# Optimization experiments

Measured on AMD Instinct MI355X. Metric: run time of the kernel, lower is better.

## Reference

```python
import jax, jax.numpy as jnp
import numpy as np

B, S, D = 8, 2048, 768        # batch, seq_len, embed_dim
G1, G2, G3 = 16, 16, 16       # grid_shape
L = 768                       # latent_dim
TEMP = 0.5                    # initial temperature (learnable scalar)
GRID_STD = 0.05               # keras 'random_normal' default stddev


def _glorot_uniform(key, fan_in, fan_out):
    lim = jnp.sqrt(6.0 / (fan_in + fan_out))
    return jax.random.uniform(key, (fan_in, fan_out), minval=-lim, maxval=lim, dtype=jnp.float32)


def setup_inputs() -> dict:
    key = jax.random.key(0)
    kx, k1, k2, k3, kg = jax.random.split(key, 5)
    x = jax.random.normal(kx, (B, S, D), dtype=jnp.float32)
    W1 = _glorot_uniform(k1, D, G1)
    W2 = _glorot_uniform(k2, D, G2)
    W3 = _glorot_uniform(k3, D, G3)
    b1 = jnp.zeros((G1,), jnp.float32)
    b2 = jnp.zeros((G2,), jnp.float32)
    b3 = jnp.zeros((G3,), jnp.float32)
    grid = GRID_STD * jax.random.normal(kg, (G1, G2, G3, L), dtype=jnp.float32)
    temperature = jnp.asarray(TEMP, dtype=jnp.float32)
    return {"x": x, "W1": W1, "b1": b1, "W2": W2, "b2": b2,
            "W3": W3, "b3": b3, "grid": grid, "temperature": temperature}


def reference(x, W1, b1, W2, b2, W3, b3, grid, temperature):
    # Flatten (batch, seq) -> tokens, process each token independently (transformer mode)
    b, s, d = x.shape
    xt = x.reshape(b * s, d)                                # (T, D)
    # Per-dimension temperature-controlled softmax addressing distributions
    p1 = jax.nn.softmax((xt @ W1 + b1) / temperature, axis=-1)   # (T, G1)
    p2 = jax.nn.softmax((xt @ W2 + b2) / temperature, axis=-1)   # (T, G2)
    p3 = jax.nn.softmax((xt @ W3 + b3) / temperature, axis=-1)   # (T, G3)
    # Joint probability (outer product) contracted with grid latent vectors:
    # out[t, l] = sum_{i,j,k} p1[t,i] p2[t,j] p3[t,k] grid[i,j,k,l]
    out = jnp.einsum('ti,tj,tk,ijkl->tl', p1, p2, p3, grid, optimize=True)
    return out.reshape(b, s, -1)                            # (B, S, L)
```

## Files before the change

kernel.cpp:

```cpp
#include <hip/hip_runtime.h>
#include <hip/hip_bf16.h>


using short8 = __attribute__((ext_vector_type(8))) short;
using f32x4  = __attribute__((ext_vector_type(4))) float;
using f32x16 = __attribute__((ext_vector_type(16))) float;
using half8  = __attribute__((ext_vector_type(8))) _Float16;
using half2v = __attribute__((ext_vector_type(2))) _Float16;
typedef unsigned short ushort_t;
typedef unsigned int uint_t;

typedef const __attribute__((address_space(1))) void* gptr_t;
typedef __attribute__((address_space(3))) void* lptr_t;

#define PSTRIDE 52

static __device__ __forceinline__ ushort_t f2h_bits(float x) {
  union { _Float16 h; ushort_t u; } c;
  c.h = (_Float16)x;
  return c.u;
}

static __device__ __forceinline__ half2v cvt_pkrtz2(float a, float b) {
  auto r = __builtin_amdgcn_cvt_pkrtz(a, b);
  union { decltype(r) i; half2v o; } u;
  u.i = r;
  return u.o;
}

__global__ __launch_bounds__(512) void k_pre(const float* __restrict__ g,
                                             ushort_t* __restrict__ gT,
                                             const float* __restrict__ x,
                                             const float* __restrict__ W1, const float* __restrict__ b1,
                                             const float* __restrict__ W2, const float* __restrict__ b2,
                                             const float* __restrict__ W3, const float* __restrict__ b3,
                                             const float* __restrict__ temp,
                                             float* __restrict__ p) {
  __shared__ union SmT {
    ushort_t tile[64][65];
    float x2[2][64][100];
    float partial[4][64][PSTRIDE];
  } sm;
  const int tid = threadIdx.x;
  const int bid = blockIdx.x;

  if (bid < 768) {
    const int r0 = (bid & 63) * 64;
    const int c0 = (bid >> 6) * 64;
#pragma unroll
    for (int it = 0; it < 2; ++it) {
      const int idx = tid + it * 512;
      const int r = idx >> 4;
      const int c = (idx & 15) << 2;
      const float4 v = *(const float4*)(g + (size_t)(r0 + r) * 768 + (c0 + c));
      sm.tile[c + 0][r] = f2h_bits(v.x);
      sm.tile[c + 1][r] = f2h_bits(v.y);
      sm.tile[c + 2][r] = f2h_bits(v.z);
      sm.tile[c + 3][r] = f2h_bits(v.w);
    }
    __syncthreads();
#pragma unroll
    for (int it = 0; it < 2; ++it) {
      const int idx = tid + it * 512;
      const int r = idx >> 4;
      const int c = (idx & 15) << 2;
      ushort4 o;
      o.x = sm.tile[r][c + 0]; o.y = sm.tile[r][c + 1];
      o.z = sm.tile[r][c + 2]; o.w = sm.tile[r][c + 3];
      *(ushort4*)(gT + (size_t)(c0 + r) * 4096 + (r0 + c)) = o;
    }
    return;
  }

  const int lane = tid & 63;
  const int wv = __builtin_amdgcn_readfirstlane(tid >> 6);
  const int t0 = (bid - 768) * 64;

  float acc[48];
#pragma unroll
  for (int q = 0; q < 48; ++q) acc[q] = 0.f;

  const float* xbase = x + (size_t)t0 * 768;
  auto load_chunk = [&](int c, int b) {
#pragma unroll
    for (int it = 0; it < 3; ++it) {
      const int q = tid + it * 512;
      const int r = q / 24;
      const int c4 = q % 24;
      const float4 v = *(const float4*)(xbase + (size_t)r * 768 + c * 96 + c4 * 4);
      *(float4*)&sm.x2[b][r][c4 * 4] = v;
    }
  };

  load_chunk(0, 0);
  __syncthreads();
  for (int c = 0; c < 8; ++c) {
    const int cur = c & 1;
    if (c < 7) load_chunk(c + 1, cur ^ 1);
    float xv[12];
#pragma unroll
    for (int rr = 0; rr < 3; ++rr) {
      const f32x4 v = *(const f32x4*)&sm.x2[cur][lane][wv * 12 + rr * 4];
      xv[rr * 4 + 0] = v[0]; xv[rr * 4 + 1] = v[1];
      xv[rr * 4 + 2] = v[2]; xv[rr * 4 + 3] = v[3];
    }
#pragma unroll
    for (int dd = 0; dd < 12; ++dd) {
      const int d = c * 96 + wv * 12 + dd;
      const float xs = xv[dd];
      const float* w1r = W1 + d * 16;
      const float* w2r = W2 + d * 16;
      const float* w3r = W3 + d * 16;
#pragma unroll
      for (int gg = 0; gg < 16; ++gg) {
        acc[gg]      = fmaf(xs, w1r[gg], acc[gg]);
        acc[16 + gg] = fmaf(xs, w2r[gg], acc[16 + gg]);
        acc[32 + gg] = fmaf(xs, w3r[gg], acc[32 + gg]);
      }
    }
    __syncthreads();
  }

  if (wv >= 4) {
    f32x4* dst = (f32x4*)sm.partial[wv - 4][lane];
#pragma unroll
    for (int q = 0; q < 12; ++q) dst[q] = *(const f32x4*)&acc[q * 4];
  }
  __syncthreads();
  if (wv < 4) {
    const f32x4* src = (const f32x4*)sm.partial[wv][lane];
#pragma unroll
    for (int q = 0; q < 12; ++q) {
      const f32x4 v = src[q];
#pragma unroll
      for (int e = 0; e < 4; ++e) acc[q * 4 + e] += v[e];
    }
  }
  __syncthreads();
  if (wv == 2 || wv == 3) {
    f32x4* dst = (f32x4*)sm.partial[wv - 2][lane];
#pragma unroll
    for (int q = 0; q < 12; ++q) dst[q] = *(const f32x4*)&acc[q * 4];
  }
  __syncthreads();
  if (wv < 2) {
    const f32x4* src = (const f32x4*)sm.partial[wv][lane];
#pragma unroll
    for (int q = 0; q < 12; ++q) {
      const f32x4 v = src[q];
#pragma unroll
      for (int e = 0; e < 4; ++e) acc[q * 4 + e] += v[e];
    }
  }
  __syncthreads();
  if (wv == 1) {
    f32x4* dst = (f32x4*)sm.partial[0][lane];
#pragma unroll
    for (int q = 0; q < 12; ++q) dst[q] = *(const f32x4*)&acc[q * 4];
  }
  __syncthreads();
  if (wv == 0) {
    const f32x4* src = (const f32x4*)sm.partial[0][lane];
#pragma unroll
    for (int q = 0; q < 12; ++q) {
      const f32x4 v = src[q];
#pragma unroll
      for (int e = 0; e < 4; ++e) acc[q * 4 + e] += v[e];
    }
    const float invT = 1.0f / temp[0];
    float* prow = p + (size_t)(t0 + lane) * PSTRIDE;
#pragma unroll
    for (int grp = 0; grp < 3; ++grp) {
      const float* bias = (grp == 0) ? b1 : (grp == 1) ? b2 : b3;
      float z[16];
      float m = -3.0e38f;
#pragma unroll
      for (int q = 0; q < 16; ++q) {
        z[q] = (acc[grp * 16 + q] + bias[q]) * invT;
        m = fmaxf(m, z[q]);
      }
      float s = 0.f;
#pragma unroll
      for (int q = 0; q < 16; ++q) { z[q] = __expf(z[q] - m); s += z[q]; }
      const float rs = 1.0f / s;
#pragma unroll
      for (int q = 0; q < 16; ++q) prow[grp * 16 + q] = z[q] * rs;
    }
  }
}

__global__ __launch_bounds__(256, 2) void k_gemm(const float* __restrict__ p_g,
                                                 const ushort_t* __restrict__ gT,
                                                 float* __restrict__ out) {
  __shared__ ushort_t Bt[2][192 * 64];
  __shared__ float p1T[16 * 128];

  const int tid = threadIdx.x;
  const int lane = tid & 63;
  const int wv = __builtin_amdgcn_readfirstlane(tid >> 6);
  const int wm = wv >> 1, wn = wv & 1;
  const int g = lane >> 5;
  const int l31 = lane & 31;

  const int f = blockIdx.y * 128 + blockIdx.x;
  const int w = (f & 7) * 64 + (f >> 3);
  const int m0 = (w & 127) * 128;
  const int n0 = (w >> 7) * 192;

  if (tid < 128) {
    const float* pr = p_g + (size_t)(m0 + tid) * PSTRIDE;
#pragma unroll
    for (int qq = 0; qq < 4; ++qq) {
      const f32x4 v = *(const f32x4*)(pr + qq * 4);
#pragma unroll
      for (int e = 0; e < 4; ++e) p1T[(qq * 4 + e) * 128 + tid] = v[e];
    }
  }

  const int rowA0 = m0 + wm * 64 + l31;
  half2v p2h[2][16];
  float p3r[2][8];
#pragma unroll
  for (int mr = 0; mr < 2; ++mr) {
    const float* pr = p_g + (size_t)(rowA0 + mr * 32) * PSTRIDE;
#pragma unroll
    for (int qq = 0; qq < 4; ++qq) {
      const f32x4 v = *(const f32x4*)(pr + 16 + qq * 4);
#pragma unroll
      for (int e = 0; e < 4; ++e)
        p2h[mr][qq * 4 + e] = cvt_pkrtz2(v[e], v[e]);
    }
#pragma unroll
    for (int qq = 0; qq < 2; ++qq) {
      const f32x4 v = *(const f32x4*)(pr + 32 + 8 * g + qq * 4);
      p3r[mr][qq * 4 + 0] = v[0]; p3r[mr][qq * 4 + 1] = v[1];
      p3r[mr][qq * 4 + 2] = v[2]; p3r[mr][qq * 4 + 3] = v[3];
    }
  }

  const int srow = wv * 48 + (lane >> 3);
  const int schunk = (lane & 7) ^ (lane >> 3);
  const ushort_t* sbase = gT + (size_t)(n0 + srow) * 4096 + schunk * 8;
  auto stage = [&](int buf, int kt) {
    const ushort_t* src = sbase + kt * 64;
#pragma unroll
    for (int q = 0; q < 6; ++q) {
      __builtin_amdgcn_global_load_lds((gptr_t)(src + (size_t)q * 8 * 4096),
                                       (lptr_t)&Bt[buf][(wv * 48 + q * 8) * 64], 16, 0, 0);
    }
  };

  f32x16 acc[2][3];
#pragma unroll
  for (int mr = 0; mr < 2; ++mr)
#pragma unroll
    for (int nf = 0; nf < 3; ++nf)
#pragma unroll
      for (int e = 0; e < 16; ++e) acc[mr][nf][e] = 0.f;

  stage(0, 0);
  asm volatile("s_waitcnt vmcnt(0) lgkmcnt(0)" ::: "memory");
  __builtin_amdgcn_s_barrier();

  const int rowLoc0 = wm * 64 + l31;
  for (int io = 0; io < 16; ++io) {
    half2v p1p3h[2][4];
#pragma unroll
    for (int mr = 0; mr < 2; ++mr) {
      const float p1v = p1T[io * 128 + rowLoc0 + mr * 32];
#pragma unroll
      for (int q = 0; q < 4; ++q)
        p1p3h[mr][q] = cvt_pkrtz2(p1v * p3r[mr][2 * q],
                                  p1v * p3r[mr][2 * q + 1]);
    }
#pragma unroll
    for (int kq = 0; kq < 4; ++kq) {
      const int kt = io * 4 + kq;
      const ushort_t* bbuf = Bt[kq & 1];

      half8 b[4][3];
#pragma unroll
      for (int s = 0; s < 4; ++s) {
        const int cd = 2 * s + g;
#pragma unroll
        for (int nf = 0; nf < 3; ++nf) {
          const int r = wn * 96 + nf * 32 + l31;
          b[s][nf] = *(const half8*)&bbuf[r * 64 + ((cd ^ (r & 7)) << 3)];
        }
      }
      if (kq < 3 || io < 15) stage((kq + 1) & 1, kt + 1);

#pragma unroll
      for (int s = 0; s < 4; ++s) {
        const int j = kq * 4 + s;
        half8 a[2];
#pragma unroll
        for (int mr = 0; mr < 2; ++mr) {
          union { half2v h2[4]; half8 h8; } pk;
#pragma unroll
          for (int q = 0; q < 4; ++q) pk.h2[q] = p2h[mr][j] * p1p3h[mr][q];
          a[mr] = pk.h8;
        }
        __builtin_amdgcn_s_setprio(1);
#pragma unroll
        for (int mr = 0; mr < 2; ++mr)
#pragma unroll
          for (int nf = 0; nf < 3; ++nf)
            acc[mr][nf] = __builtin_amdgcn_mfma_f32_32x32x16_f16(a[mr], b[s][nf], acc[mr][nf], 0, 0, 0);
        __builtin_amdgcn_s_setprio(0);
      }
      asm volatile("s_waitcnt vmcnt(0)" ::: "memory");
      __builtin_amdgcn_s_barrier();
    }
  }

#pragma unroll
  for (int mr = 0; mr < 2; ++mr)
#pragma unroll
    for (int nf = 0; nf < 3; ++nf)
#pragma unroll
      for (int reg = 0; reg < 16; ++reg) {
        const int row = (reg & 3) + 8 * (reg >> 2) + 4 * g;
        const int t = m0 + wm * 64 + mr * 32 + row;
        out[(size_t)t * 768 + n0 + wn * 96 + nf * 32 + l31] = acc[mr][nf][reg];
      }
}

extern "C" void kernel_launch(void* const* d_in, const int* in_sizes, int n_in,
                              void* d_out, int out_size, void* d_ws, size_t ws_size,
                              hipStream_t stream) {
  (void)in_sizes; (void)n_in; (void)out_size; (void)ws_size;
  const float* x    = (const float*)d_in[0];
  const float* W1   = (const float*)d_in[1];
  const float* b1   = (const float*)d_in[2];
  const float* W2   = (const float*)d_in[3];
  const float* b2   = (const float*)d_in[4];
  const float* W3   = (const float*)d_in[5];
  const float* b3   = (const float*)d_in[6];
  const float* grid = (const float*)d_in[7];
  const float* temp = (const float*)d_in[8];
  float* out = (float*)d_out;

  ushort_t* gT = (ushort_t*)d_ws;
  float* p = (float*)((char*)d_ws + 6291456);

  k_pre<<<dim3(1024), 512, 0, stream>>>(grid, gT, x, W1, b1, W2, b2, W3, b3, temp, p);
  k_gemm<<<dim3(128, 4), 256, 0, stream>>>(p, gT, out);
}
```

Before: 131.3 us.

## Triple-buffer B tiles with two-deep prefetch and vectorize projection FMAs

After: 150.3 us. +14.5%, slower.

```diff
diff --git a/kernel.cpp b/kernel.cpp
--- a/kernel.cpp
+++ b/kernel.cpp
@@ -3,6 +3,7 @@
 
 
 using short8 = __attribute__((ext_vector_type(8))) short;
+using f32x2  = __attribute__((ext_vector_type(2))) float;
 using f32x4  = __attribute__((ext_vector_type(4))) float;
 using f32x16 = __attribute__((ext_vector_type(16))) float;
 using half8  = __attribute__((ext_vector_type(8))) _Float16;
@@ -79,6 +80,7 @@
   float acc[48];
 #pragma unroll
   for (int q = 0; q < 48; ++q) acc[q] = 0.f;
+  f32x2* a2 = (f32x2*)acc;
 
   const float* xbase = x + (size_t)t0 * 768;
   auto load_chunk = [&](int c, int b) {
@@ -108,14 +110,15 @@
     for (int dd = 0; dd < 12; ++dd) {
       const int d = c * 96 + wv * 12 + dd;
       const float xs = xv[dd];
-      const float* w1r = W1 + d * 16;
-      const float* w2r = W2 + d * 16;
-      const float* w3r = W3 + d * 16;
-#pragma unroll
-      for (int gg = 0; gg < 16; ++gg) {
-        acc[gg]      = fmaf(xs, w1r[gg], acc[gg]);
-        acc[16 + gg] = fmaf(xs, w2r[gg], acc[16 + gg]);
-        acc[32 + gg] = fmaf(xs, w3r[gg], acc[32 + gg]);
+      const f32x2 xs2 = {xs, xs};
+      const f32x2* w1r = (const f32x2*)(W1 + d * 16);
+      const f32x2* w2r = (const f32x2*)(W2 + d * 16);
+      const f32x2* w3r = (const f32x2*)(W3 + d * 16);
+#pragma unroll
+      for (int gg = 0; gg < 8; ++gg) {
+        a2[gg]      = __builtin_elementwise_fma(xs2, w1r[gg], a2[gg]);
+        a2[8 + gg]  = __builtin_elementwise_fma(xs2, w2r[gg], a2[8 + gg]);
+        a2[16 + gg] = __builtin_elementwise_fma(xs2, w3r[gg], a2[16 + gg]);
       }
     }
     __syncthreads();
@@ -192,8 +195,8 @@
 __global__ __launch_bounds__(256, 2) void k_gemm(const float* __restrict__ p_g,
                                                  const ushort_t* __restrict__ gT,
                                                  float* __restrict__ out) {
-  __shared__ ushort_t Bt[2][192 * 64];
-  __shared__ float p1T[16 * 128];
+  __shared__ ushort_t Bt[3 * 192 * 64];
+  __shared__ ushort_t p1h[16 * 128];
 
   const int tid = threadIdx.x;
   const int lane = tid & 63;
@@ -213,7 +216,7 @@
     for (int qq = 0; qq < 4; ++qq) {
       const f32x4 v = *(const f32x4*)(pr + qq * 4);
 #pragma unroll
-      for (int e = 0; e < 4; ++e) p1T[(qq * 4 + e) * 128 + tid] = v[e];
+      for (int e = 0; e < 4; ++e) p1h[(qq * 4 + e) * 128 + tid] = f2h_bits(v[e]);
     }
   }
 
@@ -246,7 +249,7 @@
 #pragma unroll
     for (int q = 0; q < 6; ++q) {
       __builtin_amdgcn_global_load_lds((gptr_t)(src + (size_t)q * 8 * 4096),
-                                       (lptr_t)&Bt[buf][(wv * 48 + q * 8) * 64], 16, 0, 0);
+                                       (lptr_t)&Bt[buf * 12288 + (wv * 48 + q * 8) * 64], 16, 0, 0);
     }
   };
 
@@ -258,16 +261,24 @@
 #pragma unroll
       for (int e = 0; e < 16; ++e) acc[mr][nf][e] = 0.f;
 
-  stage(0, 0);
   asm volatile("s_waitcnt vmcnt(0) lgkmcnt(0)" ::: "memory");
   __builtin_amdgcn_s_barrier();
 
+  stage(0, 0);
+  stage(1, 1);
+  asm volatile("s_waitcnt vmcnt(6)" ::: "memory");
+  __builtin_amdgcn_s_barrier();
+
   const int rowLoc0 = wm * 64 + l31;
+  int bufc = 0;
+  int sbuf = 2;
   for (int io = 0; io < 16; ++io) {
     half2v p1p3h[2][4];
 #pragma unroll
     for (int mr = 0; mr < 2; ++mr) {
-      const float p1v = p1T[io * 128 + rowLoc0 + mr * 32];
+      union { ushort_t u; _Float16 h; } c;
+      c.u = p1h[io * 128 + rowLoc0 + mr * 32];
+      const float p1v = (float)c.h;
 #pragma unroll
       for (int q = 0; q < 4; ++q)
         p1p3h[mr][q] = cvt_pkrtz2(p1v * p3r[mr][2 * q],
@@ -276,8 +287,9 @@
 #pragma unroll
     for (int kq = 0; kq < 4; ++kq) {
       const int kt = io * 4 + kq;
-      const ushort_t* bbuf = Bt[kq & 1];
-
+      if (kt < 62) stage(sbuf, kt + 2);
+
+      const ushort_t* bbuf = &Bt[bufc * 12288];
       half8 b[4][3];
 #pragma unroll
       for (int s = 0; s < 4; ++s) {
@@ -288,7 +300,6 @@
           b[s][nf] = *(const half8*)&bbuf[r * 64 + ((cd ^ (r & 7)) << 3)];
         }
       }
-      if (kq < 3 || io < 15) stage((kq + 1) & 1, kt + 1);
 
 #pragma unroll
       for (int s = 0; s < 4; ++s) {
@@ -309,8 +320,15 @@
             acc[mr][nf] = __builtin_amdgcn_mfma_f32_32x32x16_f16(a[mr], b[s][nf], acc[mr][nf], 0, 0, 0);
         __builtin_amdgcn_s_setprio(0);
       }
-      asm volatile("s_waitcnt vmcnt(0)" ::: "memory");
-      __builtin_amdgcn_s_barrier();
+
+      if (kt < 62) {
+        asm volatile("s_waitcnt vmcnt(6)" ::: "memory");
+      } else if (kt == 62) {
+        asm volatile("s_waitcnt vmcnt(0)" ::: "memory");
+      }
+      if (kt < 63) __builtin_amdgcn_s_barrier();
+      bufc = (bufc == 2) ? 0 : bufc + 1;
+      sbuf = (sbuf == 2) ? 0 : sbuf + 1;
     }
   }
 
```

## Compute addressing logits with fp16 MFMA and split pre-pass into pack and prep kernels

Applied to the files above, without the earlier changes.

After: 106.6 us, median of 2. -18.8%, faster.

```diff
diff --git a/kernel.cpp b/kernel.cpp
--- a/kernel.cpp
+++ b/kernel.cpp
@@ -2,7 +2,7 @@
 #include <hip/hip_bf16.h>
 
 
-using short8 = __attribute__((ext_vector_type(8))) short;
+using f32x2  = __attribute__((ext_vector_type(2))) float;
 using f32x4  = __attribute__((ext_vector_type(4))) float;
 using f32x16 = __attribute__((ext_vector_type(16))) float;
 using half8  = __attribute__((ext_vector_type(8))) _Float16;
@@ -28,164 +28,126 @@
   return u.o;
 }
 
-__global__ __launch_bounds__(512) void k_pre(const float* __restrict__ g,
-                                             ushort_t* __restrict__ gT,
-                                             const float* __restrict__ x,
-                                             const float* __restrict__ W1, const float* __restrict__ b1,
-                                             const float* __restrict__ W2, const float* __restrict__ b2,
-                                             const float* __restrict__ W3, const float* __restrict__ b3,
-                                             const float* __restrict__ temp,
-                                             float* __restrict__ p) {
-  __shared__ union SmT {
-    ushort_t tile[64][65];
-    float x2[2][64][100];
-    float partial[4][64][PSTRIDE];
-  } sm;
+__global__ __launch_bounds__(256) void k_pack(const float* __restrict__ g,
+                                              ushort_t* __restrict__ gT,
+                                              const float* __restrict__ W1,
+                                              const float* __restrict__ W2,
+                                              const float* __restrict__ W3,
+                                              ushort_t* __restrict__ wfrag) {
+  const int tx = threadIdx.x;
+  if (blockIdx.y == 12) {
+    if (blockIdx.x >= 9) return;
+#pragma unroll
+    for (int j = 0; j < 16; ++j) {
+      const int u = blockIdx.x * 4096 + tx * 16 + j;
+      const int e = u & 7;
+      const int l = (u >> 3) & 63;
+      const int frag = u >> 9;
+      const int ks = frag / 3, nf = frag % 3;
+      const int d = ks * 32 + 8 * (l >> 4) + e;
+      const int col = l & 15;
+      const float* Wsel = (nf == 0) ? W1 : (nf == 1) ? W2 : W3;
+      wfrag[u] = f2h_bits(Wsel[d * 16 + col]);
+    }
+    return;
+  }
+  __shared__ ushort_t tile[64][65];
+  const int r0 = blockIdx.x * 64;
+  const int c0 = blockIdx.y * 64;
+#pragma unroll
+  for (int it = 0; it < 4; ++it) {
+    const int idx = tx + it * 256;
+    const int r = idx >> 4;
+    const int c = (idx & 15) << 2;
+    const float4 v = *(const float4*)(g + (size_t)(r0 + r) * 768 + (c0 + c));
+    tile[c + 0][r] = f2h_bits(v.x);
+    tile[c + 1][r] = f2h_bits(v.y);
+    tile[c + 2][r] = f2h_bits(v.z);
+    tile[c + 3][r] = f2h_bits(v.w);
+  }
+  __syncthreads();
+#pragma unroll
+  for (int it = 0; it < 4; ++it) {
+    const int idx = tx + it * 256;
+    const int r = idx >> 4;
+    const int c = (idx & 15) << 2;
+    ushort4 o;
+    o.x = tile[r][c + 0]; o.y = tile[r][c + 1];
+    o.z = tile[r][c + 2]; o.w = tile[r][c + 3];
+    *(ushort4*)(gT + (size_t)(c0 + r) * 4096 + (r0 + c)) = o;
+  }
+}
+
+__global__ __launch_bounds__(256) void k_prep(const float* __restrict__ x,
+                                              const ushort_t* __restrict__ wfrag,
+                                              const float* __restrict__ b1,
+                                              const float* __restrict__ b2,
+                                              const float* __restrict__ b3,
+                                              const float* __restrict__ temp,
+                                              float* __restrict__ p) {
   const int tid = threadIdx.x;
-  const int bid = blockIdx.x;
-
-  if (bid < 768) {
-    const int r0 = (bid & 63) * 64;
-    const int c0 = (bid >> 6) * 64;
-#pragma unroll
-    for (int it = 0; it < 2; ++it) {
-      const int idx = tid + it * 512;
-      const int r = idx >> 4;
-      const int c = (idx & 15) << 2;
-      const float4 v = *(const float4*)(g + (size_t)(r0 + r) * 768 + (c0 + c));
-      sm.tile[c + 0][r] = f2h_bits(v.x);
-      sm.tile[c + 1][r] = f2h_bits(v.y);
-      sm.tile[c + 2][r] = f2h_bits(v.z);
-      sm.tile[c + 3][r] = f2h_bits(v.w);
-    }
-    __syncthreads();
-#pragma unroll
-    for (int it = 0; it < 2; ++it) {
-      const int idx = tid + it * 512;
-      const int r = idx >> 4;
-      const int c = (idx & 15) << 2;
-      ushort4 o;
-      o.x = sm.tile[r][c + 0]; o.y = sm.tile[r][c + 1];
-      o.z = sm.tile[r][c + 2]; o.w = sm.tile[r][c + 3];
-      *(ushort4*)(gT + (size_t)(c0 + r) * 4096 + (r0 + c)) = o;
-    }
-    return;
-  }
-
   const int lane = tid & 63;
-  const int wv = __builtin_amdgcn_readfirstlane(tid >> 6);
-  const int t0 = (bid - 768) * 64;
-
-  float acc[48];
-#pragma unroll
-  for (int q = 0; q < 48; ++q) acc[q] = 0.f;
-
-  const float* xbase = x + (size_t)t0 * 768;
-  auto load_chunk = [&](int c, int b) {
-#pragma unroll
-    for (int it = 0; it < 3; ++it) {
-      const int q = tid + it * 512;
-      const int r = q / 24;
-      const int c4 = q % 24;
-      const float4 v = *(const float4*)(xbase + (size_t)r * 768 + c * 96 + c4 * 4);
-      *(float4*)&sm.x2[b][r][c4 * 4] = v;
-    }
-  };
-
-  load_chunk(0, 0);
-  __syncthreads();
-  for (int c = 0; c < 8; ++c) {
-    const int cur = c & 1;
-    if (c < 7) load_chunk(c + 1, cur ^ 1);
-    float xv[12];
-#pragma unroll
-    for (int rr = 0; rr < 3; ++rr) {
-      const f32x4 v = *(const f32x4*)&sm.x2[cur][lane][wv * 12 + rr * 4];
-      xv[rr * 4 + 0] = v[0]; xv[rr * 4 + 1] = v[1];
-      xv[rr * 4 + 2] = v[2]; xv[rr * 4 + 3] = v[3];
-    }
-#pragma unroll
-    for (int dd = 0; dd < 12; ++dd) {
-      const int d = c * 96 + wv * 12 + dd;
-      const float xs = xv[dd];
-      const float* w1r = W1 + d * 16;
-      const float* w2r = W2 + d * 16;
-      const float* w3r = W3 + d * 16;
-#pragma unroll
-      for (int gg = 0; gg < 16; ++gg) {
-        acc[gg]      = fmaf(xs, w1r[gg], acc[gg]);
-        acc[16 + gg] = fmaf(xs, w2r[gg], acc[16 + gg]);
-        acc[32 + gg] = fmaf(xs, w3r[gg], acc[32 + gg]);
-      }
-    }
-    __syncthreads();
-  }
-
-  if (wv >= 4) {
-    f32x4* dst = (f32x4*)sm.partial[wv - 4][lane];
-#pragma unroll
-    for (int q = 0; q < 12; ++q) dst[q] = *(const f32x4*)&acc[q * 4];
-  }
-  __syncthreads();
-  if (wv < 4) {
-    const f32x4* src = (const f32x4*)sm.partial[wv][lane];
-#pragma unroll
-    for (int q = 0; q < 12; ++q) {
-      const f32x4 v = src[q];
-#pragma unroll
-      for (int e = 0; e < 4; ++e) acc[q * 4 + e] += v[e];
-    }
-  }
-  __syncthreads();
-  if (wv == 2 || wv == 3) {
-    f32x4* dst = (f32x4*)sm.partial[wv - 2][lane];
-#pragma unroll
-    for (int q = 0; q < 12; ++q) dst[q] = *(const f32x4*)&acc[q * 4];
-  }
-  __syncthreads();
-  if (wv < 2) {
-    const f32x4* src = (const f32x4*)sm.partial[wv][lane];
-#pragma unroll
-    for (int q = 0; q < 12; ++q) {
-      const f32x4 v = src[q];
-#pragma unroll
-      for (int e = 0; e < 4; ++e) acc[q * 4 + e] += v[e];
-    }
-  }
-  __syncthreads();
-  if (wv == 1) {
-    f32x4* dst = (f32x4*)sm.partial[0][lane];
-#pragma unroll
-    for (int q = 0; q < 12; ++q) dst[q] = *(const f32x4*)&acc[q * 4];
-  }
-  __syncthreads();
-  if (wv == 0) {
-    const f32x4* src = (const f32x4*)sm.partial[0][lane];
-#pragma unroll
-    for (int q = 0; q < 12; ++q) {
-      const f32x4 v = src[q];
-#pragma unroll
-      for (int e = 0; e < 4; ++e) acc[q * 4 + e] += v[e];
-    }
-    const float invT = 1.0f / temp[0];
-    float* prow = p + (size_t)(t0 + lane) * PSTRIDE;
-#pragma unroll
-    for (int grp = 0; grp < 3; ++grp) {
-      const float* bias = (grp == 0) ? b1 : (grp == 1) ? b2 : b3;
-      float z[16];
-      float m = -3.0e38f;
-#pragma unroll
-      for (int q = 0; q < 16; ++q) {
-        z[q] = (acc[grp * 16 + q] + bias[q]) * invT;
-        m = fmaxf(m, z[q]);
-      }
-      float s = 0.f;
-#pragma unroll
-      for (int q = 0; q < 16; ++q) { z[q] = __expf(z[q] - m); s += z[q]; }
-      const float rs = 1.0f / s;
-#pragma unroll
-      for (int q = 0; q < 16; ++q) prow[grp * 16 + q] = z[q] * rs;
-    }
+  const int wv = tid >> 6;
+  const int t0w = blockIdx.x * 64 + wv * 16;
+  const int m = lane & 15;
+  const int q = lane >> 4;
+
+  const float* xrow = x + (size_t)(t0w + m) * 768 + q * 8;
+
+  f32x4 acc[3];
+#pragma unroll
+  for (int nf = 0; nf < 3; ++nf) acc[nf] = (f32x4){0.f, 0.f, 0.f, 0.f};
+
+  const ushort_t* wf = wfrag + lane * 8;
+#pragma unroll
+  for (int ks = 0; ks < 24; ++ks) {
+    const f32x4 xa = *(const f32x4*)(xrow + ks * 32);
+    const f32x4 xb = *(const f32x4*)(xrow + ks * 32 + 4);
+    union { half2v h2[4]; half8 h8; } pk;
+    pk.h2[0] = cvt_pkrtz2(xa[0], xa[1]);
+    pk.h2[1] = cvt_pkrtz2(xa[2], xa[3]);
+    pk.h2[2] = cvt_pkrtz2(xb[0], xb[1]);
+    pk.h2[3] = cvt_pkrtz2(xb[2], xb[3]);
+    const half8 a = pk.h8;
+#pragma unroll
+    for (int nf = 0; nf < 3; ++nf) {
+      const half8 w = *(const half8*)&wf[(size_t)(ks * 3 + nf) * 512];
+      acc[nf] = __builtin_amdgcn_mfma_f32_16x16x32_f16(a, w, acc[nf], 0, 0, 0);
+    }
+  }
+
+  const float invT = 1.0f / temp[0];
+  float z[3][4];
+  const float bias[3] = {b1[m], b2[m], b3[m]};
+#pragma unroll
+  for (int nf = 0; nf < 3; ++nf)
+#pragma unroll
+    for (int r = 0; r < 4; ++r) z[nf][r] = (acc[nf][r] + bias[nf]) * invT;
+
+#pragma unroll
+  for (int grp = 0; grp < 3; ++grp) {
+    float mx[4], sm[4];
+#pragma unroll
+    for (int r = 0; r < 4; ++r) mx[r] = z[grp][r];
+#pragma unroll
+    for (int msk = 1; msk < 16; msk <<= 1)
+#pragma unroll
+      for (int r = 0; r < 4; ++r) mx[r] = fmaxf(mx[r], __shfl_xor(mx[r], msk));
+#pragma unroll
+    for (int r = 0; r < 4; ++r) { z[grp][r] = __expf(z[grp][r] - mx[r]); sm[r] = z[grp][r]; }
+#pragma unroll
+    for (int msk = 1; msk < 16; msk <<= 1)
+#pragma unroll
+      for (int r = 0; r < 4; ++r) sm[r] += __shfl_xor(sm[r], msk);
+#pragma unroll
+    for (int r = 0; r < 4; ++r) z[grp][r] /= sm[r];
+  }
+
+#pragma unroll
+  for (int r = 0; r < 4; ++r) {
+    float* prow = p + (size_t)(t0w + 4 * q + r) * PSTRIDE + m;
+#pragma unroll
+    for (int grp = 0; grp < 3; ++grp) prow[grp * 16] = z[grp][r];
   }
 }
 
@@ -244,9 +206,9 @@
   auto stage = [&](int buf, int kt) {
     const ushort_t* src = sbase + kt * 64;
 #pragma unroll
-    for (int q = 0; q < 6; ++q) {
-      __builtin_amdgcn_global_load_lds((gptr_t)(src + (size_t)q * 8 * 4096),
-                                       (lptr_t)&Bt[buf][(wv * 48 + q * 8) * 64], 16, 0, 0);
+    for (int qq = 0; qq < 6; ++qq) {
+      __builtin_amdgcn_global_load_lds((gptr_t)(src + (size_t)qq * 8 * 4096),
+                                       (lptr_t)&Bt[buf][(wv * 48 + qq * 8) * 64], 16, 0, 0);
     }
   };
 
@@ -269,9 +231,9 @@
     for (int mr = 0; mr < 2; ++mr) {
       const float p1v = p1T[io * 128 + rowLoc0 + mr * 32];
 #pragma unroll
-      for (int q = 0; q < 4; ++q)
-        p1p3h[mr][q] = cvt_pkrtz2(p1v * p3r[mr][2 * q],
-                                  p1v * p3r[mr][2 * q + 1]);
+      for (int qq = 0; qq < 4; ++qq)
+        p1p3h[mr][qq] = cvt_pkrtz2(p1v * p3r[mr][2 * qq],
+                                   p1v * p3r[mr][2 * qq + 1]);
     }
 #pragma unroll
     for (int kq = 0; kq < 4; ++kq) {
@@ -298,7 +260,7 @@
         for (int mr = 0; mr < 2; ++mr) {
           union { half2v h2[4]; half8 h8; } pk;
 #pragma unroll
-          for (int q = 0; q < 4; ++q) pk.h2[q] = p2h[mr][j] * p1p3h[mr][q];
+          for (int qq = 0; qq < 4; ++qq) pk.h2[qq] = p2h[mr][j] * p1p3h[mr][qq];
           a[mr] = pk.h8;
         }
         __builtin_amdgcn_s_setprio(1);
@@ -343,7 +305,9 @@
 
   ushort_t* gT = (ushort_t*)d_ws;
   float* p = (float*)((char*)d_ws + 6291456);
-
-  k_pre<<<dim3(1024), 512, 0, stream>>>(grid, gT, x, W1, b1, W2, b2, W3, b3, temp, p);
+  ushort_t* wfrag = (ushort_t*)((char*)d_ws + 6291456 + 3407872);
+
+  k_pack<<<dim3(64, 13), 256, 0, stream>>>(grid, gT, W1, W2, W3, wfrag);
+  k_prep<<<dim3(256), 256, 0, stream>>>(x, wfrag, b1, b2, b3, temp, p);
   k_gemm<<<dim3(128, 4), 256, 0, stream>>>(p, gT, out);
 }
```
